# Kernel tuning notes

Measured on AMD Instinct MI355X. Metric: run time of the kernel, lower is better.

Reference implementation:

```python
import jax, jax.numpy as jnp
import numpy as np

N = 100000
E = 3200000
IN_C = 128
HID = 16
OUT_C = 16
EA = 16


def setup_inputs() -> dict:
    key = jax.random.key(0)
    ks = jax.random.split(key, 8)
    x = jax.random.normal(ks[0], (N, IN_C), dtype=jnp.float32)
    edge_index = jax.random.randint(ks[1], (2, E), 0, N, dtype=jnp.int32)
    edge_attr = jax.random.normal(ks[2], (E, EA), dtype=jnp.float32)
    We = jax.random.normal(ks[3], (EA, HID), dtype=jnp.float32) * (1.0 / np.sqrt(EA))
    be = jnp.zeros((HID,), dtype=jnp.float32)
    W1 = jax.random.normal(ks[4], (IN_C, HID), dtype=jnp.float32) * (1.0 / np.sqrt(IN_C))
    b1 = jnp.zeros((HID,), dtype=jnp.float32)
    W2 = jax.random.normal(ks[5], (HID, OUT_C), dtype=jnp.float32) * (1.0 / np.sqrt(HID))
    b2 = jnp.zeros((OUT_C,), dtype=jnp.float32)
    return {"x": x, "edge_index": edge_index, "edge_attr": edge_attr,
            "We": We, "be": be, "W1": W1, "b1": b1, "W2": W2, "b2": b2}


def _gcn_conv(h, src, dst, ew, dinv_src, dinv_dst, dinv_sq, W, b):
    # h: [N, Cin] -> transform first (PyG order), then normalized gather-scatter.
    h = h @ W                                   # [N, C], C == HID == OUT_C == 16
    norm = dinv_src * ew * dinv_dst             # [E, 16] per-edge per-channel norm
    msg = norm * h[src]                          # gather + fuse edge weight
    agg = jax.ops.segment_sum(msg, dst, num_segments=N)  # scatter-add
    agg = agg + dinv_sq * h                      # self-loop (weight 1) contribution
    return agg + b


def reference(x, edge_index, edge_attr, We, be, W1, b1, W2, b2):
    src, dst = edge_index[0], edge_index[1]
    ew = edge_attr @ We + be                     # [E, 16] edge weights (per channel)
    # symmetric degree normalization with self loops (weight 1), per channel
    deg = jax.ops.segment_sum(ew, dst, num_segments=N) + 1.0  # [N, 16]
    dinv = jnp.where(deg > 0, jax.lax.rsqrt(jnp.abs(deg) + 1e-12), 0.0)
    dinv_src = dinv[src]
    dinv_dst = dinv[dst]
    dinv_sq = dinv * dinv
    h = jax.nn.relu(_gcn_conv(x, src, dst, ew, dinv_src, dinv_dst, dinv_sq, W1, b1))
    # dropout is identity in eval mode
    out = _gcn_conv(h, src, dst, ew, dinv_src, dinv_dst, dinv_sq, W2, b2)
    return out
```

## Files before the change

### kernel.cpp

```cpp
#include <hip/hip_runtime.h>

static constexpr int N_NODES = 100000;
static constexpr int N_EDGES = 3200000;
static constexpr int NC16    = N_NODES * 16;
static constexpr int RB      = 256;
static constexpr int NB      = (N_NODES + RB - 1) / RB;
static constexpr int CAP     = 9000;
static constexpr int EPB     = 8192;
static constexpr int NPB     = (N_EDGES + EPB - 1) / EPB;

__device__ __forceinline__ float4 v4fma(float s, float4 w, float4 acc) {
    acc.x = fmaf(s, w.x, acc.x);
    acc.y = fmaf(s, w.y, acc.y);
    acc.z = fmaf(s, w.z, acc.z);
    acc.w = fmaf(s, w.w, acc.w);
    return acc;
}

template<int KK>
__device__ __forceinline__ float4 qbcast(float4 a) {
    constexpr int ctrl = KK * 0x55;
    float4 r;
    r.x = __int_as_float(__builtin_amdgcn_mov_dpp(__float_as_int(a.x), ctrl, 0xF, 0xF, true));
    r.y = __int_as_float(__builtin_amdgcn_mov_dpp(__float_as_int(a.y), ctrl, 0xF, 0xF, true));
    r.z = __int_as_float(__builtin_amdgcn_mov_dpp(__float_as_int(a.z), ctrl, 0xF, 0xF, true));
    r.w = __int_as_float(__builtin_amdgcn_mov_dpp(__float_as_int(a.w), ctrl, 0xF, 0xF, true));
    return r;
}

template<int KK>
__device__ __forceinline__ float4 ewstep(float4 a, const float4* wc, float4 ew) {
    float4 v = qbcast<KK>(a);
    ew = v4fma(v.x, wc[4*KK + 0], ew);
    ew = v4fma(v.y, wc[4*KK + 1], ew);
    ew = v4fma(v.z, wc[4*KK + 2], ew);
    ew = v4fma(v.w, wc[4*KK + 3], ew);
    return ew;
}

__global__ __launch_bounds__(256)
void k_zero(int* g) {
    int t = blockIdx.x * 256 + threadIdx.x;
    if (t < NB) g[t] = 0;
}


__global__ __launch_bounds__(256)
void k_part(const int* __restrict__ srcI, const int* __restrict__ dstI,
            int* __restrict__ gcount, int2* __restrict__ meta)
{
    __shared__ int hist[NB];
    const int tid  = threadIdx.x;
    const int e0   = blockIdx.x * EPB;
    const int ecnt = min(EPB, N_EDGES - e0);
    for (int t = tid; t < NB; t += 256) hist[t] = 0;
    __syncthreads();
    for (int i = tid; i < ecnt; i += 256) {
        int d = dstI[e0 + i];
        atomicAdd(&hist[d >> 8], 1);
    }
    __syncthreads();
    for (int t = tid; t < NB; t += 256) {
        int h = hist[t];
        hist[t] = (h > 0) ? atomicAdd(&gcount[t], h) : 0;
    }
    __syncthreads();
    for (int i = tid; i < ecnt; i += 256) {
        int e = e0 + i;
        int d = dstI[e];
        int s = srcI[e];
        int b = d >> 8;
        int pos = atomicAdd(&hist[b], 1);
        if (pos < CAP)
            meta[b * CAP + pos] = make_int2(e, (s << 8) | (d & 255));
    }
}

template<bool HAS_P>
__global__ __launch_bounds__(512)
void k_bucket(const float* __restrict__ ea, const int2* __restrict__ meta,
              const int* __restrict__ gcount, const float* __restrict__ We,
              const float* __restrict__ be, const float* __restrict__ p,
              float* __restrict__ acc)
{
    __shared__ double accS[RB * 16];
    const int tid = threadIdx.x;
    const int b   = blockIdx.x;
    for (int t = tid; t < RB * 16; t += 512) accS[t] = 0.0;

    const int c4 = tid & 3;
    float4 wc[16];
    const float4* We4 = (const float4*)We;
#pragma unroll
    for (int k = 0; k < 16; ++k) wc[k] = We4[k * 4 + c4];
    const float4 bev = ((const float4*)be)[c4];
    const int cnt = min(gcount[b], CAP);
    const int2* ml = meta + b * CAP;
    const float4* ea4 = (const float4*)ea;
    const float4* p4  = (const float4*)p;
    __syncthreads();

#pragma unroll 2
    for (int i = tid >> 2; i < cnt; i += 128) {
        int2 m = ml[i];
        float4 a = ea4[m.x * 4 + c4];
        float4 pv;
        if (HAS_P) pv = p4[((unsigned)m.y >> 8) * 4 + c4];
        const int dl = m.y & 255;
        float4 ew = bev;
        ew = ewstep<0>(a, wc, ew);
        ew = ewstep<1>(a, wc, ew);
        ew = ewstep<2>(a, wc, ew);
        ew = ewstep<3>(a, wc, ew);
        double* o = accS + dl * 16 + c4 * 4;
        if (HAS_P) {
            atomicAdd(o + 0, (double)(ew.x * pv.x));
            atomicAdd(o + 1, (double)(ew.y * pv.y));
            atomicAdd(o + 2, (double)(ew.z * pv.z));
            atomicAdd(o + 3, (double)(ew.w * pv.w));
        } else {
            atomicAdd(o + 0, (double)ew.x);
            atomicAdd(o + 1, (double)ew.y);
            atomicAdd(o + 2, (double)ew.z);
            atomicAdd(o + 3, (double)ew.w);
        }
    }
    __syncthreads();

    for (int t = tid; t < RB * 4; t += 512) {
        int nl = t >> 2;
        int ng = b * RB + nl;
        if (ng < N_NODES) {
            const double* s = accS + nl * 16 + (t & 3) * 4;
            float4 o;
            o.x = (float)s[0]; o.y = (float)s[1];
            o.z = (float)s[2]; o.w = (float)s[3];
            ((float4*)acc)[ng * 4 + (t & 3)] = o;
        }
    }
}

__global__ __launch_bounds__(256)
void k_dinv(float* dd) {
    int t = blockIdx.x * 256 + threadIdx.x;
    if (t < NC16) {
        float d = dd[t] + 1.0f;
        dd[t] = (d > 0.0f) ? rsqrtf(d + 1e-12f) : 0.0f;
    }
}

__global__ __launch_bounds__(256)
void k_xw1(const float* __restrict__ x, const float* __restrict__ W1,
           const float* __restrict__ dinv, float* __restrict__ p)
{
    __shared__ float4 w1s[512];
    const int t = threadIdx.x;
    const float4* W14 = (const float4*)W1;
    w1s[t]       = W14[t];
    w1s[t + 256] = W14[t + 256];
    __syncthreads();

    const int c4 = t & 3;
    const int nl = t >> 2;
    const int nb = blockIdx.x * 256;
    int node[4];
    float4 acc[4];
#pragma unroll
    for (int i = 0; i < 4; ++i) {
        node[i] = nb + i * 64 + nl;
        acc[i]  = make_float4(0.f, 0.f, 0.f, 0.f);
    }
    const float4* x4 = (const float4*)x;

    for (int k4 = 0; k4 < 32; ++k4) {
        float4 wv0 = w1s[(k4 * 4 + 0) * 4 + c4];
        float4 wv1 = w1s[(k4 * 4 + 1) * 4 + c4];
        float4 wv2 = w1s[(k4 * 4 + 2) * 4 + c4];
        float4 wv3 = w1s[(k4 * 4 + 3) * 4 + c4];
#pragma unroll
        for (int i = 0; i < 4; ++i) {
            int nn = node[i] < N_NODES ? node[i] : (N_NODES - 1);
            float4 xv = x4[nn * 32 + k4];
            acc[i] = v4fma(xv.x, wv0, acc[i]);
            acc[i] = v4fma(xv.y, wv1, acc[i]);
            acc[i] = v4fma(xv.z, wv2, acc[i]);
            acc[i] = v4fma(xv.w, wv3, acc[i]);
        }
    }
    const float4* dinv4 = (const float4*)dinv;
    float4* pp = (float4*)p;
#pragma unroll
    for (int i = 0; i < 4; ++i) {
        if (node[i] < N_NODES) {
            float4 dv = dinv4[node[i] * 4 + c4];
            float4 o;
            o.x = dv.x * acc[i].x; o.y = dv.y * acc[i].y;
            o.z = dv.z * acc[i].z; o.w = dv.w * acc[i].w;
            pp[node[i] * 4 + c4] = o;
        }
    }
}

__global__ __launch_bounds__(256)
void k_mid(const float* __restrict__ accA, const float* __restrict__ dinv,
           const float* __restrict__ W2, const float* __restrict__ b1,
           float* __restrict__ p)
{
    const int tid = blockIdx.x * 256 + threadIdx.x;
    const int q   = tid >> 2;
    if (q >= N_NODES) return;
    const int c4 = threadIdx.x & 3;

    float4 wc[16];
    const float4* W24 = (const float4*)W2;
#pragma unroll
    for (int k = 0; k < 16; ++k) wc[k] = W24[k * 4 + c4];
    const float4 b1v = ((const float4*)b1)[c4];

    const float4 av = ((const float4*)accA)[q * 4 + c4];
    const float4 pv = ((const float4*)p)[q * 4 + c4];
    const float4 dv = ((const float4*)dinv)[q * 4 + c4];

    float4 h1;
    h1.x = fmaxf(fmaf(dv.x, av.x + pv.x, b1v.x), 0.f);
    h1.y = fmaxf(fmaf(dv.y, av.y + pv.y, b1v.y), 0.f);
    h1.z = fmaxf(fmaf(dv.z, av.z + pv.z, b1v.z), 0.f);
    h1.w = fmaxf(fmaf(dv.w, av.w + pv.w, b1v.w), 0.f);

    float4 h2 = make_float4(0.f, 0.f, 0.f, 0.f);
    h2 = ewstep<0>(h1, wc, h2);
    h2 = ewstep<1>(h1, wc, h2);
    h2 = ewstep<2>(h1, wc, h2);
    h2 = ewstep<3>(h1, wc, h2);

    float4 o;
    o.x = dv.x * h2.x; o.y = dv.y * h2.y;
    o.z = dv.z * h2.z; o.w = dv.w * h2.w;
    ((float4*)p)[q * 4 + c4] = o;
}

__global__ __launch_bounds__(256)
void k_out(const float* __restrict__ accB, const float* __restrict__ dinv,
           const float* __restrict__ p, const float* __restrict__ b2,
           float* __restrict__ out)
{
    const int tid = blockIdx.x * 256 + threadIdx.x;
    const int q   = tid >> 2;
    if (q >= N_NODES) return;
    const int c4 = threadIdx.x & 3;
    const float4 b2v = ((const float4*)b2)[c4];
    const float4 av = ((const float4*)accB)[q * 4 + c4];
    const float4 pv = ((const float4*)p)[q * 4 + c4];
    const float4 dv = ((const float4*)dinv)[q * 4 + c4];
    float4 o;
    o.x = fmaf(dv.x, av.x + pv.x, b2v.x);
    o.y = fmaf(dv.y, av.y + pv.y, b2v.y);
    o.z = fmaf(dv.z, av.z + pv.z, b2v.z);
    o.w = fmaf(dv.w, av.w + pv.w, b2v.w);
    ((float4*)out)[q * 4 + c4] = o;
}

extern "C" void kernel_launch(void* const* d_in, const int* in_sizes, int n_in,
                              void* d_out, int out_size, void* d_ws, size_t ws_size,
                              hipStream_t stream)
{
    const float* x   = (const float*)d_in[0];
    const int*   ei  = (const int*)d_in[1];
    const float* ea  = (const float*)d_in[2];
    const float* We  = (const float*)d_in[3];
    const float* be  = (const float*)d_in[4];
    const float* W1  = (const float*)d_in[5];
    const float* b1  = (const float*)d_in[6];
    const float* W2  = (const float*)d_in[7];
    const float* b2  = (const float*)d_in[8];
    float* out = (float*)d_out;

    const int* srcI = ei;
    const int* dstI = ei + N_EDGES;

    float* dinv = (float*)d_ws;
    float* p    = dinv + NC16;
    float* accA = p + NC16;
    float* accB = accA + NC16;
    int2*  meta = (int2*)(accB + NC16);
    int*   gcount = (int*)(meta + (size_t)NB * CAP);

    const dim3 blk(256);
    hipLaunchKernelGGL(k_zero, dim3((NB + 255) / 256), blk, 0, stream, gcount);
    hipLaunchKernelGGL(k_part, dim3(NPB), blk, 0, stream, srcI, dstI, gcount, meta);
    hipLaunchKernelGGL((k_bucket<false>), dim3(NB), dim3(512), 0, stream,
                       ea, meta, gcount, We, be, (const float*)nullptr, dinv);
    hipLaunchKernelGGL(k_dinv, dim3(NC16 / 256), blk, 0, stream, dinv);
    hipLaunchKernelGGL(k_xw1, dim3((N_NODES + 255) / 256), blk, 0, stream, x, W1, dinv, p);
    hipLaunchKernelGGL((k_bucket<true>), dim3(NB), dim3(512), 0, stream,
                       ea, meta, gcount, We, be, p, accA);
    hipLaunchKernelGGL(k_mid, dim3((N_NODES * 4 + 255) / 256), blk, 0, stream,
                       accA, dinv, W2, b1, p);
    hipLaunchKernelGGL((k_bucket<true>), dim3(NB), dim3(512), 0, stream,
                       ea, meta, gcount, We, be, p, accB);
    hipLaunchKernelGGL(k_out, dim3((N_NODES * 4 + 255) / 256), blk, 0, stream,
                       accB, dinv, p, b2, out);
}
```

Measured before the change: 680.0 us.

## Precompute per-edge weights into bucketed records and reuse across passes

Computes edge weights once while partitioning edges into destination buckets, storing them contiguously with packed src/dst metadata. The degree and both aggregation passes then read these records sequentially instead of re-gathering edge_attr and recomputing the 16x16 projection. This trades a large extra workspace write (about 240 MB) for contiguous reads and less recomputation. A fallback keeps the old path when the workspace is too small.

After: 693.2 us. About the same (+1.9%).

```diff
diff --git a/kernel.cpp b/kernel.cpp
--- a/kernel.cpp
+++ b/kernel.cpp
@@ -44,6 +44,142 @@
     if (t < NB) g[t] = 0;
 }
 
+__global__ __launch_bounds__(512)
+void k_part_ew(const int* __restrict__ srcI, const int* __restrict__ dstI,
+               const float* __restrict__ ea, const float* __restrict__ We,
+               const float* __restrict__ be,
+               int* __restrict__ gcount,
+               float4* __restrict__ ewRec4, int* __restrict__ metaRec)
+{
+    __shared__ int hist[NB];
+    const int tid  = threadIdx.x;
+    const int e0   = blockIdx.x * EPB;
+    const int ecnt = min(EPB, N_EDGES - e0);
+    for (int t = tid; t < NB; t += 512) hist[t] = 0;
+    __syncthreads();
+    for (int i = tid; i < ecnt; i += 512) {
+        int d = dstI[e0 + i];
+        atomicAdd(&hist[d >> 8], 1);
+    }
+    __syncthreads();
+    for (int t = tid; t < NB; t += 512) {
+        int h = hist[t];
+        hist[t] = (h > 0) ? atomicAdd(&gcount[t], h) : 0;
+    }
+    __syncthreads();
+
+    const int c4 = tid & 3;
+    float4 wc[16];
+    const float4* We4 = (const float4*)We;
+#pragma unroll
+    for (int k = 0; k < 16; ++k) wc[k] = We4[k * 4 + c4];
+    const float4 bev = ((const float4*)be)[c4];
+    const float4* ea4 = (const float4*)ea;
+
+    for (int i = tid >> 2; i < ecnt; i += 128) {
+        const int e = e0 + i;
+        const int d = dstI[e];
+        const int s = srcI[e];
+        const int b = d >> 8;
+        float4 a = ea4[e * 4 + c4];
+        float4 ew = bev;
+        ew = ewstep<0>(a, wc, ew);
+        ew = ewstep<1>(a, wc, ew);
+        ew = ewstep<2>(a, wc, ew);
+        ew = ewstep<3>(a, wc, ew);
+        int pos = 0;
+        if (c4 == 0) pos = atomicAdd(&hist[b], 1);
+        pos = __shfl(pos, (threadIdx.x & 63) & ~3, 64);
+        if (pos < CAP) {
+            const int r = b * CAP + pos;
+            ewRec4[r * 4 + c4] = ew;
+            if (c4 == 0) metaRec[r] = (s << 8) | (d & 255);
+        }
+    }
+}
+
+__global__ __launch_bounds__(512)
+void k_degdinv(const float4* __restrict__ ewRec4, const int* __restrict__ metaRec,
+               const int* __restrict__ gcount, float* __restrict__ dinv)
+{
+    __shared__ double accS[RB * 16];
+    const int tid = threadIdx.x;
+    const int b   = blockIdx.x;
+    for (int t = tid; t < RB * 16; t += 512) accS[t] = 0.0;
+    const int c4  = tid & 3;
+    const int cnt = min(gcount[b], CAP);
+    const int base = b * CAP;
+    __syncthreads();
+
+#pragma unroll 2
+    for (int i = tid >> 2; i < cnt; i += 128) {
+        float4 ew = ewRec4[(base + i) * 4 + c4];
+        int m = metaRec[base + i];
+        int dl = m & 255;
+        double* o = accS + dl * 16 + c4 * 4;
+        atomicAdd(o + 0, (double)ew.x);
+        atomicAdd(o + 1, (double)ew.y);
+        atomicAdd(o + 2, (double)ew.z);
+        atomicAdd(o + 3, (double)ew.w);
+    }
+    __syncthreads();
+
+    for (int t = tid; t < RB * 4; t += 512) {
+        int nl = t >> 2;
+        int ng = b * RB + nl;
+        if (ng < N_NODES) {
+            const double* s = accS + nl * 16 + (t & 3) * 4;
+            float4 o;
+            float d0 = (float)s[0] + 1.0f; o.x = (d0 > 0.f) ? rsqrtf(d0 + 1e-12f) : 0.f;
+            float d1 = (float)s[1] + 1.0f; o.y = (d1 > 0.f) ? rsqrtf(d1 + 1e-12f) : 0.f;
+            float d2 = (float)s[2] + 1.0f; o.z = (d2 > 0.f) ? rsqrtf(d2 + 1e-12f) : 0.f;
+            float d3 = (float)s[3] + 1.0f; o.w = (d3 > 0.f) ? rsqrtf(d3 + 1e-12f) : 0.f;
+            ((float4*)dinv)[ng * 4 + (t & 3)] = o;
+        }
+    }
+}
+
+__global__ __launch_bounds__(512)
+void k_gather(const float4* __restrict__ ewRec4, const int* __restrict__ metaRec,
+              const int* __restrict__ gcount, const float* __restrict__ p,
+              float* __restrict__ acc)
+{
+    __shared__ double accS[RB * 16];
+    const int tid = threadIdx.x;
+    const int b   = blockIdx.x;
+    for (int t = tid; t < RB * 16; t += 512) accS[t] = 0.0;
+    const int c4  = tid & 3;
+    const int cnt = min(gcount[b], CAP);
+    const int base = b * CAP;
+    const float4* p4 = (const float4*)p;
+    __syncthreads();
+
+#pragma unroll 2
+    for (int i = tid >> 2; i < cnt; i += 128) {
+        float4 ew = ewRec4[(base + i) * 4 + c4];
+        int m = metaRec[base + i];
+        float4 pv = p4[((unsigned)m >> 8) * 4 + c4];
+        int dl = m & 255;
+        double* o = accS + dl * 16 + c4 * 4;
+        atomicAdd(o + 0, (double)(ew.x * pv.x));
+        atomicAdd(o + 1, (double)(ew.y * pv.y));
+        atomicAdd(o + 2, (double)(ew.z * pv.z));
+        atomicAdd(o + 3, (double)(ew.w * pv.w));
+    }
+    __syncthreads();
+
+    for (int t = tid; t < RB * 4; t += 512) {
+        int nl = t >> 2;
+        int ng = b * RB + nl;
+        if (ng < N_NODES) {
+            const double* s = accS + nl * 16 + (t & 3) * 4;
+            float4 o;
+            o.x = (float)s[0]; o.y = (float)s[1];
+            o.z = (float)s[2]; o.w = (float)s[3];
+            ((float4*)acc)[ng * 4 + (t & 3)] = o;
+        }
+    }
+}
 
 __global__ __launch_bounds__(256)
 void k_part(const int* __restrict__ srcI, const int* __restrict__ dstI,
@@ -282,22 +418,51 @@
     float* p    = dinv + NC16;
     float* accA = p + NC16;
     float* accB = accA + NC16;
-    int2*  meta = (int2*)(accB + NC16);
-    int*   gcount = (int*)(meta + (size_t)NB * CAP);
+
+    const size_t needA = (size_t)4 * NC16 * 4
+                       + (size_t)NB * CAP * (sizeof(float4) * 4 + sizeof(int))
+                       + (size_t)NB * sizeof(int) + 4096;
 
     const dim3 blk(256);
-    hipLaunchKernelGGL(k_zero, dim3((NB + 255) / 256), blk, 0, stream, gcount);
-    hipLaunchKernelGGL(k_part, dim3(NPB), blk, 0, stream, srcI, dstI, gcount, meta);
-    hipLaunchKernelGGL((k_bucket<false>), dim3(NB), dim3(512), 0, stream,
-                       ea, meta, gcount, We, be, (const float*)nullptr, dinv);
-    hipLaunchKernelGGL(k_dinv, dim3(NC16 / 256), blk, 0, stream, dinv);
-    hipLaunchKernelGGL(k_xw1, dim3((N_NODES + 255) / 256), blk, 0, stream, x, W1, dinv, p);
-    hipLaunchKernelGGL((k_bucket<true>), dim3(NB), dim3(512), 0, stream,
-                       ea, meta, gcount, We, be, p, accA);
-    hipLaunchKernelGGL(k_mid, dim3((N_NODES * 4 + 255) / 256), blk, 0, stream,
-                       accA, dinv, W2, b1, p);
-    hipLaunchKernelGGL((k_bucket<true>), dim3(NB), dim3(512), 0, stream,
-                       ea, meta, gcount, We, be, p, accB);
-    hipLaunchKernelGGL(k_out, dim3((N_NODES * 4 + 255) / 256), blk, 0, stream,
-                       accB, dinv, p, b2, out);
-}
+
+    if (ws_size >= needA) {
+        float4* ewRec4 = (float4*)(accB + NC16);
+        int*    metaRec = (int*)(ewRec4 + (size_t)NB * CAP * 4);
+        int*    gcount  = metaRec + (size_t)NB * CAP;
+
+        hipLaunchKernelGGL(k_zero, dim3((NB + 255) / 256), blk, 0, stream, gcount);
+        hipLaunchKernelGGL(k_part_ew, dim3(NPB), dim3(512), 0, stream,
+                           srcI, dstI, ea, We, be, gcount, ewRec4, metaRec);
+        hipLaunchKernelGGL(k_degdinv, dim3(NB), dim3(512), 0, stream,
+                           ewRec4, metaRec, gcount, dinv);
+        hipLaunchKernelGGL(k_xw1, dim3((N_NODES + 255) / 256), blk, 0, stream,
+                           x, W1, dinv, p);
+        hipLaunchKernelGGL(k_gather, dim3(NB), dim3(512), 0, stream,
+                           ewRec4, metaRec, gcount, p, accA);
+        hipLaunchKernelGGL(k_mid, dim3((N_NODES * 4 + 255) / 256), blk, 0, stream,
+                           accA, dinv, W2, b1, p);
+        hipLaunchKernelGGL(k_gather, dim3(NB), dim3(512), 0, stream,
+                           ewRec4, metaRec, gcount, p, accB);
+        hipLaunchKernelGGL(k_out, dim3((N_NODES * 4 + 255) / 256), blk, 0, stream,
+                           accB, dinv, p, b2, out);
+    } else {
+        int2* meta   = (int2*)(accB + NC16);
+        int*  gcount = (int*)(meta + (size_t)NB * CAP);
+
+        hipLaunchKernelGGL(k_zero, dim3((NB + 255) / 256), blk, 0, stream, gcount);
+        hipLaunchKernelGGL(k_part, dim3(NPB), blk, 0, stream, srcI, dstI, gcount, meta);
+        hipLaunchKernelGGL((k_bucket<false>), dim3(NB), dim3(512), 0, stream,
+                           ea, meta, gcount, We, be, (const float*)nullptr, dinv);
+        hipLaunchKernelGGL(k_dinv, dim3(NC16 / 256), blk, 0, stream, dinv);
+        hipLaunchKernelGGL(k_xw1, dim3((N_NODES + 255) / 256), blk, 0, stream,
+                           x, W1, dinv, p);
+        hipLaunchKernelGGL((k_bucket<true>), dim3(NB), dim3(512), 0, stream,
+                           ea, meta, gcount, We, be, p, accA);
+        hipLaunchKernelGGL(k_mid, dim3((N_NODES * 4 + 255) / 256), blk, 0, stream,
+                           accA, dinv, W2, b1, p);
+        hipLaunchKernelGGL((k_bucket<true>), dim3(NB), dim3(512), 0, stream,
+                           ea, meta, gcount, We, be, p, accB);
+        hipLaunchKernelGGL(k_out, dim3((N_NODES * 4 + 255) / 256), blk, 0, stream,
+                           accB, dinv, p, b2, out);
+    }
+}
```

## Halve bucket size, swizzle LDS double accumulators, fuse dinv into degree pass

Applied to the files above, without the earlier changes.

Halves the destination bucket size (256 to 128 nodes) so there are twice as many bucket blocks. This gives more parallelism and halves the shared-memory double accumulator per block, which should raise occupancy. Partitioning now runs as 512 blocks of 1024 threads. The LDS atomic slot for each channel is rotated by the local node index to spread bank conflicts. The separate dinv kernel is removed by computing rsqrt in the epilogue of the degree bucket pass. The smaller CAP (4800) raises the risk of silently dropping edges if any 128-node bucket receives more than 4800 edges (the expected count is about 4096).

Result: no change. 682.2 us (+0.3%).

```diff
diff --git a/kernel.cpp b/kernel.cpp
--- a/kernel.cpp
+++ b/kernel.cpp
@@ -3,11 +3,11 @@
 static constexpr int N_NODES = 100000;
 static constexpr int N_EDGES = 3200000;
 static constexpr int NC16    = N_NODES * 16;
-static constexpr int RB      = 256;
+static constexpr int RB      = 128;
 static constexpr int NB      = (N_NODES + RB - 1) / RB;
-static constexpr int CAP     = 9000;
-static constexpr int EPB     = 8192;
-static constexpr int NPB     = (N_EDGES + EPB - 1) / EPB;
+static constexpr int CAP     = 4800;
+static constexpr int NPB     = 512;
+static constexpr int EPB     = (N_EDGES + NPB - 1) / NPB;
 
 __device__ __forceinline__ float4 v4fma(float s, float4 w, float4 acc) {
     acc.x = fmaf(s, w.x, acc.x);
@@ -38,14 +38,23 @@
     return ew;
 }
 
+__device__ __forceinline__ void accum4(double* __restrict__ accS, int dl, int c4,
+                                       double v0, double v1, double v2, double v3) {
+    double* row = accS + dl * 16;
+    const int pb = (c4 * 4 + dl) & 15;
+    atomicAdd(row + ((pb + 0) & 15), v0);
+    atomicAdd(row + ((pb + 1) & 15), v1);
+    atomicAdd(row + ((pb + 2) & 15), v2);
+    atomicAdd(row + ((pb + 3) & 15), v3);
+}
+
 __global__ __launch_bounds__(256)
 void k_zero(int* g) {
     int t = blockIdx.x * 256 + threadIdx.x;
     if (t < NB) g[t] = 0;
 }
 
-
-__global__ __launch_bounds__(256)
+__global__ __launch_bounds__(1024)
 void k_part(const int* __restrict__ srcI, const int* __restrict__ dstI,
             int* __restrict__ gcount, int2* __restrict__ meta)
 {
@@ -53,35 +62,35 @@
     const int tid  = threadIdx.x;
     const int e0   = blockIdx.x * EPB;
     const int ecnt = min(EPB, N_EDGES - e0);
-    for (int t = tid; t < NB; t += 256) hist[t] = 0;
-    __syncthreads();
-    for (int i = tid; i < ecnt; i += 256) {
+    for (int t = tid; t < NB; t += 1024) hist[t] = 0;
+    __syncthreads();
+    for (int i = tid; i < ecnt; i += 1024) {
         int d = dstI[e0 + i];
-        atomicAdd(&hist[d >> 8], 1);
-    }
-    __syncthreads();
-    for (int t = tid; t < NB; t += 256) {
+        atomicAdd(&hist[d >> 7], 1);
+    }
+    __syncthreads();
+    for (int t = tid; t < NB; t += 1024) {
         int h = hist[t];
         hist[t] = (h > 0) ? atomicAdd(&gcount[t], h) : 0;
     }
     __syncthreads();
-    for (int i = tid; i < ecnt; i += 256) {
+    for (int i = tid; i < ecnt; i += 1024) {
         int e = e0 + i;
         int d = dstI[e];
         int s = srcI[e];
-        int b = d >> 8;
+        int b = d >> 7;
         int pos = atomicAdd(&hist[b], 1);
         if (pos < CAP)
-            meta[b * CAP + pos] = make_int2(e, (s << 8) | (d & 255));
-    }
-}
-
-template<bool HAS_P>
+            meta[b * CAP + pos] = make_int2(e, (s << 7) | (d & 127));
+    }
+}
+
+template<int MODE>
 __global__ __launch_bounds__(512)
 void k_bucket(const float* __restrict__ ea, const int2* __restrict__ meta,
               const int* __restrict__ gcount, const float* __restrict__ We,
               const float* __restrict__ be, const float* __restrict__ p,
-              float* __restrict__ acc)
+              float* __restrict__ outv)
 {
     __shared__ double accS[RB * 16];
     const int tid = threadIdx.x;
@@ -105,24 +114,19 @@
         int2 m = ml[i];
         float4 a = ea4[m.x * 4 + c4];
         float4 pv;
-        if (HAS_P) pv = p4[((unsigned)m.y >> 8) * 4 + c4];
-        const int dl = m.y & 255;
+        if (MODE == 1) pv = p4[((unsigned)m.y >> 7) * 4 + c4];
+        const int dl = m.y & 127;
         float4 ew = bev;
         ew = ewstep<0>(a, wc, ew);
         ew = ewstep<1>(a, wc, ew);
         ew = ewstep<2>(a, wc, ew);
         ew = ewstep<3>(a, wc, ew);
-        double* o = accS + dl * 16 + c4 * 4;
-        if (HAS_P) {
-            atomicAdd(o + 0, (double)(ew.x * pv.x));
-            atomicAdd(o + 1, (double)(ew.y * pv.y));
-            atomicAdd(o + 2, (double)(ew.z * pv.z));
-            atomicAdd(o + 3, (double)(ew.w * pv.w));
+        if (MODE == 1) {
+            accum4(accS, dl, c4,
+                   (double)(ew.x * pv.x), (double)(ew.y * pv.y),
+                   (double)(ew.z * pv.z), (double)(ew.w * pv.w));
         } else {
-            atomicAdd(o + 0, (double)ew.x);
-            atomicAdd(o + 1, (double)ew.y);
-            atomicAdd(o + 2, (double)ew.z);
-            atomicAdd(o + 3, (double)ew.w);
+            accum4(accS, dl, c4, (double)ew.x, (double)ew.y, (double)ew.z, (double)ew.w);
         }
     }
     __syncthreads();
@@ -131,21 +135,22 @@
         int nl = t >> 2;
         int ng = b * RB + nl;
         if (ng < N_NODES) {
-            const double* s = accS + nl * 16 + (t & 3) * 4;
+            const double* s = accS + nl * 16;
+            const int pb = ((t & 3) * 4 + nl) & 15;
             float4 o;
-            o.x = (float)s[0]; o.y = (float)s[1];
-            o.z = (float)s[2]; o.w = (float)s[3];
-            ((float4*)acc)[ng * 4 + (t & 3)] = o;
+            if (MODE == 0) {
+                float d0 = (float)s[(pb + 0) & 15] + 1.0f; o.x = (d0 > 0.f) ? rsqrtf(d0 + 1e-12f) : 0.f;
+                float d1 = (float)s[(pb + 1) & 15] + 1.0f; o.y = (d1 > 0.f) ? rsqrtf(d1 + 1e-12f) : 0.f;
+                float d2 = (float)s[(pb + 2) & 15] + 1.0f; o.z = (d2 > 0.f) ? rsqrtf(d2 + 1e-12f) : 0.f;
+                float d3 = (float)s[(pb + 3) & 15] + 1.0f; o.w = (d3 > 0.f) ? rsqrtf(d3 + 1e-12f) : 0.f;
+            } else {
+                o.x = (float)s[(pb + 0) & 15];
+                o.y = (float)s[(pb + 1) & 15];
+                o.z = (float)s[(pb + 2) & 15];
+                o.w = (float)s[(pb + 3) & 15];
+            }
+            ((float4*)outv)[ng * 4 + (t & 3)] = o;
         }
-    }
-}
-
-__global__ __launch_bounds__(256)
-void k_dinv(float* dd) {
-    int t = blockIdx.x * 256 + threadIdx.x;
-    if (t < NC16) {
-        float d = dd[t] + 1.0f;
-        dd[t] = (d > 0.0f) ? rsqrtf(d + 1e-12f) : 0.0f;
     }
 }
 
@@ -287,16 +292,17 @@
 
     const dim3 blk(256);
     hipLaunchKernelGGL(k_zero, dim3((NB + 255) / 256), blk, 0, stream, gcount);
-    hipLaunchKernelGGL(k_part, dim3(NPB), blk, 0, stream, srcI, dstI, gcount, meta);
-    hipLaunchKernelGGL((k_bucket<false>), dim3(NB), dim3(512), 0, stream,
+    hipLaunchKernelGGL(k_part, dim3(NPB), dim3(1024), 0, stream,
+                       srcI, dstI, gcount, meta);
+    hipLaunchKernelGGL((k_bucket<0>), dim3(NB), dim3(512), 0, stream,
                        ea, meta, gcount, We, be, (const float*)nullptr, dinv);
-    hipLaunchKernelGGL(k_dinv, dim3(NC16 / 256), blk, 0, stream, dinv);
-    hipLaunchKernelGGL(k_xw1, dim3((N_NODES + 255) / 256), blk, 0, stream, x, W1, dinv, p);
-    hipLaunchKernelGGL((k_bucket<true>), dim3(NB), dim3(512), 0, stream,
+    hipLaunchKernelGGL(k_xw1, dim3((N_NODES + 255) / 256), blk, 0, stream,
+                       x, W1, dinv, p);
+    hipLaunchKernelGGL((k_bucket<1>), dim3(NB), dim3(512), 0, stream,
                        ea, meta, gcount, We, be, p, accA);
     hipLaunchKernelGGL(k_mid, dim3((N_NODES * 4 + 255) / 256), blk, 0, stream,
                        accA, dinv, W2, b1, p);
-    hipLaunchKernelGGL((k_bucket<true>), dim3(NB), dim3(512), 0, stream,
+    hipLaunchKernelGGL((k_bucket<1>), dim3(NB), dim3(512), 0, stream,
                        ea, meta, gcount, We, be, p, accB);
     hipLaunchKernelGGL(k_out, dim3((N_NODES * 4 + 255) / 256), blk, 0, stream,
                        accB, dinv, p, b2, out);
```
